# Optimization experiments

Measured on AMD Instinct MI355X. Metric: run time of the kernel, lower is better.

The kernel has to match this reference:

```python
import jax, jax.numpy as jnp
import numpy as np

B = 128   # batch_size (number of trees / source tweets)
H = 100   # tweet_out_size == GRU hidden == GAT feature dim


def _gru_layer(x, h0, Wih, Whh, bih, bhh):
    # x: [T, N, D] time-major; PyTorch GRU cell math
    def step(h, xt):
        gi = xt @ Wih.T + bih
        gh = h @ Whh.T + bhh
        ir, iz, in_ = jnp.split(gi, 3, axis=-1)
        hr, hz, hn = jnp.split(gh, 3, axis=-1)
        r = jax.nn.sigmoid(ir + hr)
        z = jax.nn.sigmoid(iz + hz)
        n = jnp.tanh(in_ + r * hn)
        h = (1.0 - z) * n + z * h
        return h, h
    hT, ys = jax.lax.scan(step, h0, x)
    return ys, hT


def _gru2(x, h0, Wih0, Whh0, bih0, bhh0, Wih1, Whh1, bih1, bhh1):
    y0, _ = _gru_layer(x, h0[0], Wih0, Whh0, bih0, bhh0)
    _, h1 = _gru_layer(y0, h0[1], Wih1, Whh1, bih1, bhh1)
    return h1  # final hidden of top layer: [N, H]


def _gat(x, ei, W, a_src, a_dst, b, heads, outc, concat):
    # PyG GATConv (eval mode, add_self_loops=True, leaky_relu slope 0.2)
    N = x.shape[0]
    loops = jnp.arange(N, dtype=ei.dtype)
    src = jnp.concatenate([ei[0], loops])
    dst = jnp.concatenate([ei[1], loops])
    h = (x @ W.T).reshape(N, heads, outc)           # [N, H, C]
    es = (h * a_src).sum(-1)                         # [N, H]
    ed = (h * a_dst).sum(-1)
    e = jax.nn.leaky_relu(es[src] + ed[dst], negative_slope=0.2)  # [E, H]
    m = jax.lax.stop_gradient(jax.ops.segment_max(e, dst, num_segments=N))
    ee = jnp.exp(e - m[dst])
    s = jax.ops.segment_sum(ee, dst, num_segments=N)
    alpha = ee / s[dst]
    out = jax.ops.segment_sum(h[src] * alpha[:, :, None], dst, num_segments=N)
    out = out.reshape(N, heads * outc) if concat else out.mean(axis=1)
    return out + b


def _forward(fl, user_text, gnode, gei, tnode, tei, idx):
    (user_feats, h0g, h0t, temb,
     gWih0, gWhh0, gbih0, gbhh0, gWih1, gWhh1, gbih1, gbhh1,
     tWih0, tWhh0, tbih0, tbhh0, tWih1, tWhh1, tbih1, tbhh1,
     uW1, ub1, uW2, ub2,
     gc1W, gc1as, gc1ad, gc1b, gc2W, gc2as, gc2ad, gc2b,
     tc1W, tc1as, tc1ad, tc1b, tc2W, tc2as, tc2ad, tc2b,
     fcW, fcb) = fl
    # --- graphGAT branch ---
    ue = jax.nn.relu(user_feats @ uW1.T + ub1) @ uW2.T + ub2        # [Nu, 100]
    ge = temb[gnode].transpose(1, 0, 2)                              # [T, Ntg, 100]
    hg = _gru2(ge, h0g, gWih0, gWhh0, gbih0, gbhh0, gWih1, gWhh1, gbih1, gbhh1)
    xg = jnp.concatenate([hg[:B], ue, hg[B:]], axis=0)               # [Ng, 100]
    xg = jax.nn.relu(_gat(xg, gei, gc1W, gc1as, gc1ad, gc1b, 8, 64, True))
    xg = jax.nn.relu(_gat(xg, gei, gc2W, gc2as, gc2ad, gc2b, 1, 100, False))
    # --- TreeGAT branch ---
    te = temb[tnode].transpose(1, 0, 2)                              # [T, Ntree, 100]
    ht = _gru2(te, h0t, tWih0, tWhh0, tbih0, tbhh0, tWih1, tWhh1, tbih1, tbhh1)
    xt = ht.at[:B].set(xg[:B])                                       # root rows <- user_root_embed
    xt = jax.nn.relu(_gat(xt, tei, tc1W, tc1as, tc1ad, tc1b, 8, 100, True))
    xt = jax.nn.relu(_gat(xt, tei, tc2W, tc2as, tc2ad, tc2b, 1, 100, False))
    # --- scatter_mean over trees + classifier ---
    ssum = jax.ops.segment_sum(xt, idx, num_segments=B)
    cnt = jax.ops.segment_sum(jnp.ones((xt.shape[0],), xt.dtype), idx, num_segments=B)
    mean = ssum / jnp.maximum(cnt, 1.0)[:, None]
    return mean @ fcW.T + fcb                                        # [B, 4]


def setup_inputs():
    key = jax.random.key(0)
    it = iter(jax.random.split(key, 60))
    def nrm(shape, s):
        return (jax.random.normal(next(it), shape) * s).astype(jnp.float32)
    Ntg, Nu, Ntree = 10000, 20000, 30000
    Ng = Ntg + Nu
    Eg, Et, V, T = 200000, 60000, 50000, 20
    inp = {}
    inp["user_text"] = jax.random.randint(next(it), (Nu, 10), 0, 1000)
    inp["user_feats"] = nrm((Nu, 9), 1.0)
    inp["graph_node_features"] = jax.random.randint(next(it), (Ntg, T), 0, V)
    inp["graph_edge_index"] = jax.random.randint(next(it), (2, Eg), 0, Ng)
    inp["merged_tree_feature"] = jax.random.randint(next(it), (Ntree, T), 0, V)
    inp["merged_tree_edge_index"] = jax.random.randint(next(it), (2, Et), 0, Ntree)
    inp["indices"] = jax.random.randint(next(it), (Ntree,), 0, B)
    inp["h0_graph"] = nrm((2, Ntg, H), 1.0)
    inp["h0_tree"] = nrm((2, Ntree, H), 1.0)
    inp["tweet_emb"] = nrm((V, H), 1.0)
    s = 0.1
    for p in ("g", "t"):
        for l in ("0", "1"):
            inp[p + "Wih" + l] = nrm((3 * H, H), s)
            inp[p + "Whh" + l] = nrm((3 * H, H), s)
            inp[p + "bih" + l] = jnp.zeros((3 * H,), jnp.float32)
            inp[p + "bhh" + l] = jnp.zeros((3 * H,), jnp.float32)
    inp["uW1"] = nrm((100, 9), s);    inp["ub1"] = jnp.zeros((100,), jnp.float32)
    inp["uW2"] = nrm((100, 100), s);  inp["ub2"] = jnp.zeros((100,), jnp.float32)
    inp["gc1W"] = nrm((512, 100), s); inp["gc1as"] = nrm((8, 64), s); inp["gc1ad"] = nrm((8, 64), s); inp["gc1b"] = jnp.zeros((512,), jnp.float32)
    inp["gc2W"] = nrm((100, 512), s); inp["gc2as"] = nrm((1, 100), s); inp["gc2ad"] = nrm((1, 100), s); inp["gc2b"] = jnp.zeros((100,), jnp.float32)
    inp["tc1W"] = nrm((800, 100), s); inp["tc1as"] = nrm((8, 100), s); inp["tc1ad"] = nrm((8, 100), s); inp["tc1b"] = jnp.zeros((800,), jnp.float32)
    inp["tc2W"] = nrm((100, 800), s); inp["tc2as"] = nrm((1, 100), s); inp["tc2ad"] = nrm((1, 100), s); inp["tc2b"] = jnp.zeros((100,), jnp.float32)
    inp["fcW"] = nrm((4, 100), s);    inp["fcb"] = jnp.zeros((4,), jnp.float32)
    return inp


def reference(user_text, user_feats, graph_node_features, graph_edge_index,
              merged_tree_feature, merged_tree_edge_index, indices,
              h0_graph, h0_tree, tweet_emb,
              gWih0, gWhh0, gbih0, gbhh0, gWih1, gWhh1, gbih1, gbhh1,
              tWih0, tWhh0, tbih0, tbhh0, tWih1, tWhh1, tbih1, tbhh1,
              uW1, ub1, uW2, ub2,
              gc1W, gc1as, gc1ad, gc1b, gc2W, gc2as, gc2ad, gc2b,
              tc1W, tc1as, tc1ad, tc1b, tc2W, tc2as, tc2ad, tc2b,
              fcW, fcb):
    fl = (user_feats, h0_graph, h0_tree, tweet_emb,
          gWih0, gWhh0, gbih0, gbhh0, gWih1, gWhh1, gbih1, gbhh1,
          tWih0, tWhh0, tbih0, tbhh0, tWih1, tWhh1, tbih1, tbhh1,
          uW1, ub1, uW2, ub2,
          gc1W, gc1as, gc1ad, gc1b, gc2W, gc2as, gc2ad, gc2b,
          tc1W, tc1as, tc1ad, tc1b, tc2W, tc2as, tc2ad, tc2b,
          fcW, fcb)
    return _forward(fl, user_text, graph_node_features, graph_edge_index,
                    merged_tree_feature, merged_tree_edge_index, indices)
```

## Files before the change

kernel.cpp:

```cpp
#include <hip/hip_runtime.h>

#define NB    128
#define HD    100
#define NU    20000
#define NTG   10000
#define NTREE 30000
#define NG    30000
#define TT    20
#define EG    200000
#define ET    60000
#define VOC   50000

#define ESTR2 448
#define WROWS 336

typedef unsigned short u16;
typedef unsigned int   u32;
typedef __attribute__((ext_vector_type(8))) short short8;
typedef __attribute__((ext_vector_type(4))) float floatx4;

__device__ __forceinline__ float sigmoidf_(float x) {
    return __fdividef(1.f, 1.f + __expf(-x));
}
__device__ __forceinline__ float tanhf_(float x) {
    return 1.f - __fdividef(2.f, __expf(2.f * x) + 1.f);
}
__device__ __forceinline__ u16 f2bf(float f) {
    u32 u = __float_as_uint(f);
    u32 r = (u + 0x7fffu + ((u >> 16) & 1u)) >> 16;
    return (u16)r;
}
__device__ __forceinline__ u16 f2bf_c(float f) {
    u32 r;
    asm("v_cvt_pk_bf16_f32 %0, %1, %2" : "=v"(r) : "v"(f), "v"(f));
    return (u16)r;
}
__device__ __forceinline__ float bf2f(u16 h) {
    return __uint_as_float(((u32)h) << 16);
}

struct GruProb {
    const u16*   Etab;
    const int*   nodes;
    const float* h0;
    const u16*   Whh0;
    const u16*   Wih1;
    const u16*   Whh1;
    u16*         hout;
    int          M;
};

__global__ __launch_bounds__(448, 2) void gru_fused9(GruProb Pg, GruProb Pt, int gblocks)
{
    const bool isg = (int)blockIdx.x < gblocks;
    const GruProb P = isg ? Pg : Pt;
    const int bx = isg ? blockIdx.x : blockIdx.x - gblocks;
    const int M  = P.M;
    const int m0 = bx * 32;

    __shared__ u16 H0[2][32 * 128];
    __shared__ u16 H1[2][32 * 128];
    __shared__ int NID[TT * 32];

    const int tid  = threadIdx.x;
    const int w    = tid >> 6, lane = tid & 63;
    const int fr   = lane & 15, quad = lane >> 4;
    const int c    = w * 16 + fr;
    const bool cok = (c < HD);

    short8 Bh0[3][4], Bx1[3][4], Bh1[3][4];
#pragma unroll
    for (int g = 0; g < 3; ++g) {
        const size_t rb = (size_t)((g * 7 + w) * 16 + fr) * 128 + quad * 8;
#pragma unroll
        for (int kk = 0; kk < 4; ++kk) {
            Bh0[g][kk] = *(const short8*)(P.Whh0 + rb + kk * 32);
            Bx1[g][kk] = *(const short8*)(P.Wih1 + rb + kk * 32);
            Bh1[g][kk] = *(const short8*)(P.Whh1 + rb + kk * 32);
        }
    }

    for (int i = tid; i < 32 * 128; i += 448) {
        H0[0][i] = 0; H0[1][i] = 0; H1[0][i] = 0; H1[1][i] = 0;
    }
    for (int i = tid; i < 32 * TT; i += 448) {
        int row = i / TT, t = i - row * TT;
        int gm = m0 + row;
        NID[t * 32 + row] = (gm < M) ? P.nodes[(size_t)gm * TT + t] : 0;
    }
    __syncthreads();
    if (tid < 32) {
        int off = 200 ^ ((tid & 7) << 4);
        *(u16*)((char*)&H0[0][0] + tid * 256 + off) = 0x3F80;
        *(u16*)((char*)&H0[1][0] + tid * 256 + off) = 0x3F80;
        *(u16*)((char*)&H1[0][0] + tid * 256 + off) = 0x3F80;
        *(u16*)((char*)&H1[1][0] + tid * 256 + off) = 0x3F80;
    }

    float h0f[2][4] = {{0.f,0.f,0.f,0.f},{0.f,0.f,0.f,0.f}};
    float h1f[2][4] = {{0.f,0.f,0.f,0.f},{0.f,0.f,0.f,0.f}};
    if (cok) {
#pragma unroll
        for (int rt = 0; rt < 2; ++rt)
#pragma unroll
        for (int r = 0; r < 4; ++r) {
            int row = rt * 16 + quad * 4 + r;
            int gm  = m0 + row;
            float v0 = 0.f, v1 = 0.f;
            if (gm < M) {
                v0 = P.h0[(size_t)gm * HD + c];
                v1 = P.h0[(size_t)(M + gm) * HD + c];
            }
            h0f[rt][r] = v0; h1f[rt][r] = v1;
            int off = (2 * c) ^ ((row & 7) << 4);
            *(u16*)((char*)&H0[0][0] + row * 256 + off) = f2bf_c(v0);
            *(u16*)((char*)&H1[0][0] + row * 256 + off) = f2bf_c(v1);
        }
    }

    u32 xlo[2][4], xhi[2][4];
    auto xpref = [&](int tn) {
        if (cok) {
#pragma unroll
            for (int rt = 0; rt < 2; ++rt)
#pragma unroll
            for (int r = 0; r < 4; ++r) {
                int row = rt * 16 + quad * 4 + r;
                int nd  = NID[tn * 32 + row];
                uint2 v = *(const uint2*)(P.Etab + (size_t)nd * ESTR2 + c * 4);
                xlo[rt][r] = v.x; xhi[rt][r] = v.y;
            }
        }
    };
    __syncthreads();
    xpref(0);

#pragma unroll
    for (int rt = 0; rt < 2; ++rt) {
        short8 a[4];
#pragma unroll
        for (int kk = 0; kk < 4; ++kk) {
            int row = rt * 16 + fr;
            int off = (kk * 64 + quad * 16) ^ ((row & 7) << 4);
            a[kk] = *(const short8*)((const char*)&H0[0][0] + row * 256 + off);
        }
        floatx4 ag[3];
#pragma unroll
        for (int g = 0; g < 3; ++g) ag[g] = (floatx4){0.f, 0.f, 0.f, 0.f};
#pragma unroll
        for (int g = 0; g < 3; ++g)
#pragma unroll
            for (int kk = 0; kk < 4; ++kk)
                ag[g] = __builtin_amdgcn_mfma_f32_16x16x32_bf16(a[kk], Bh0[g][kk], ag[g], 0, 0, 0);
        if (cok) {
#pragma unroll
            for (int r = 0; r < 4; ++r) {
                int row = rt * 16 + quad * 4 + r;
                float rr = sigmoidf_(bf2f((u16)xlo[rt][r]) + ag[0][r]);
                float zz = sigmoidf_(bf2f((u16)(xlo[rt][r] >> 16)) + ag[1][r]);
                float nn = tanhf_(bf2f((u16)xhi[rt][r]) + rr * ag[2][r]);
                float o  = (1.f - zz) * nn + zz * h0f[rt][r];
                h0f[rt][r] = o;
                *(u16*)((char*)&H0[1][0] + row * 256 + ((2 * c) ^ ((row & 7) << 4))) = f2bf_c(o);
            }
        }
    }
    __syncthreads();

    for (int r = 0; r < TT; ++r) {
        const bool doA = (r + 1 < TT);
        if (doA) xpref(r + 1);

        const char* rd0 = (const char*)&H0[(r + 1) & 1][0];
        const char* rd1 = (const char*)&H1[r & 1][0];
        char*       wr0 = (char*)&H0[r & 1][0];
        char*       wr1 = (char*)&H1[(r + 1) & 1][0];

#pragma unroll
        for (int rt = 0; rt < 2; ++rt) {
            short8 a0[4], a1[4];
#pragma unroll
            for (int kk = 0; kk < 4; ++kk) {
                int row = rt * 16 + fr;
                int off = (kk * 64 + quad * 16) ^ ((row & 7) << 4);
                a0[kk] = *(const short8*)(rd0 + row * 256 + off);
                a1[kk] = *(const short8*)(rd1 + row * 256 + off);
            }
            floatx4 rz0 = {0.f,0.f,0.f,0.f}, rz1 = {0.f,0.f,0.f,0.f};
            floatx4 xnv = {0.f,0.f,0.f,0.f}, hnv = {0.f,0.f,0.f,0.f};
#pragma unroll
            for (int kk = 0; kk < 4; ++kk)
                rz0 = __builtin_amdgcn_mfma_f32_16x16x32_bf16(a0[kk], Bx1[0][kk], rz0, 0, 0, 0);
#pragma unroll
            for (int kk = 0; kk < 4; ++kk)
                rz0 = __builtin_amdgcn_mfma_f32_16x16x32_bf16(a1[kk], Bh1[0][kk], rz0, 0, 0, 0);
#pragma unroll
            for (int kk = 0; kk < 4; ++kk)
                rz1 = __builtin_amdgcn_mfma_f32_16x16x32_bf16(a0[kk], Bx1[1][kk], rz1, 0, 0, 0);
#pragma unroll
            for (int kk = 0; kk < 4; ++kk)
                rz1 = __builtin_amdgcn_mfma_f32_16x16x32_bf16(a1[kk], Bh1[1][kk], rz1, 0, 0, 0);
#pragma unroll
            for (int kk = 0; kk < 4; ++kk)
                xnv = __builtin_amdgcn_mfma_f32_16x16x32_bf16(a0[kk], Bx1[2][kk], xnv, 0, 0, 0);
#pragma unroll
            for (int kk = 0; kk < 4; ++kk)
                hnv = __builtin_amdgcn_mfma_f32_16x16x32_bf16(a1[kk], Bh1[2][kk], hnv, 0, 0, 0);
            floatx4 ag[3];
#pragma unroll
            for (int g = 0; g < 3; ++g) ag[g] = (floatx4){0.f, 0.f, 0.f, 0.f};
            if (doA) {
#pragma unroll
                for (int g = 0; g < 3; ++g)
#pragma unroll
                    for (int kk = 0; kk < 4; ++kk)
                        ag[g] = __builtin_amdgcn_mfma_f32_16x16x32_bf16(a0[kk], Bh0[g][kk], ag[g], 0, 0, 0);
            }
            if (cok) {
#pragma unroll
                for (int r4 = 0; r4 < 4; ++r4) {
                    int row = rt * 16 + quad * 4 + r4;
                    float rr = sigmoidf_(rz0[r4]);
                    float zz = sigmoidf_(rz1[r4]);
                    float nn = tanhf_(xnv[r4] + rr * hnv[r4]);
                    float o  = (1.f - zz) * nn + zz * h1f[rt][r4];
                    h1f[rt][r4] = o;
                    *(u16*)(wr1 + row * 256 + ((2 * c) ^ ((row & 7) << 4))) = f2bf_c(o);
                }
                if (doA) {
#pragma unroll
                    for (int r4 = 0; r4 < 4; ++r4) {
                        int row = rt * 16 + quad * 4 + r4;
                        float rr = sigmoidf_(bf2f((u16)xlo[rt][r4]) + ag[0][r4]);
                        float zz = sigmoidf_(bf2f((u16)(xlo[rt][r4] >> 16)) + ag[1][r4]);
                        float nn = tanhf_(bf2f((u16)xhi[rt][r4]) + rr * ag[2][r4]);
                        float o  = (1.f - zz) * nn + zz * h0f[rt][r4];
                        h0f[rt][r4] = o;
                        *(u16*)(wr0 + row * 256 + ((2 * c) ^ ((row & 7) << 4))) = f2bf_c(o);
                    }
                }
            }
        }
        __syncthreads();
    }

    for (int i = tid; i < 32 * 128; i += 448) {
        int row = i >> 7, cc = i & 127;
        int gm = m0 + row;
        if (gm < M) {
            int off = (2 * cc) ^ ((row & 7) << 4);
            P.hout[(size_t)gm * 128 + cc] = *(const u16*)((const char*)&H1[0][0] + row * 256 + off);
        }
    }
}

#define LDST 40
__global__ __launch_bounds__(256) void gemm_mfma(
    const u16* __restrict__ A, const u16* __restrict__ B,
    float* __restrict__ Cf, u16* __restrict__ Cb,
    int M, int N, int Kt, int lda, int ldw, int ldc, int ileave)
{
    const int m0 = blockIdx.x * 64;
    if (m0 >= M) return;
    const int n0 = blockIdx.y * 64;

    __shared__ u16 Als[64 * LDST];
    __shared__ u16 Wls[64 * LDST];

    const int tid  = threadIdx.x;
    const int wave = tid >> 6, lane = tid & 63;
    const int row  = tid >> 2, part = (tid & 3) * 8;
    const int fr   = lane & 15, quad = lane >> 4;

    floatx4 acc[4];
#pragma unroll
    for (int t = 0; t < 4; ++t) acc[t] = (floatx4){0.f, 0.f, 0.f, 0.f};

    const int am = m0 + row;  const bool aok = am < M;
    const int wn = n0 + row;  const bool wok = wn < N;
    const uint4 z4 = {0u, 0u, 0u, 0u};

    for (int kk = 0; kk < Kt; ++kk) {
        uint4 av = aok ? *(const uint4*)(A + (size_t)am * lda + kk * 32 + part) : z4;
        uint4 wv = wok ? *(const uint4*)(B + (size_t)wn * ldw + kk * 32 + part) : z4;
        __syncthreads();
        *(uint4*)&Als[row * LDST + part] = av;
        *(uint4*)&Wls[row * LDST + part] = wv;
        __syncthreads();
        short8 af = *(const short8*)&Als[((wave << 4) + fr) * LDST + quad * 8];
#pragma unroll
        for (int t = 0; t < 4; ++t) {
            short8 bf = *(const short8*)&Wls[((t << 4) + fr) * LDST + quad * 8];
            acc[t] = __builtin_amdgcn_mfma_f32_16x16x32_bf16(af, bf, acc[t], 0, 0, 0);
        }
    }

    const int orow0 = m0 + (wave << 4) + quad * 4;
#pragma unroll
    for (int t = 0; t < 4; ++t) {
        int col = n0 + (t << 4) + fr;
        if (col >= N) continue;
#pragma unroll
        for (int r = 0; r < 4; ++r) {
            int mr = orow0 + r;
            if (mr >= M) continue;
            float v = acc[t][r];
            if (Cf) Cf[(size_t)mr * ldc + col] = v;
            if (Cb) {
                if (ileave) {
                    int g = col / 100, cc = col - g * 100;
                    Cb[(size_t)mr * ESTR2 + cc * 4 + g] = f2bf(v);
                } else {
                    Cb[(size_t)mr * ldc + col] = f2bf(v);
                }
            }
        }
    }
}

__global__ __launch_bounds__(256) void gemm_nt(
    const float* __restrict__ A, const float* __restrict__ W,
    const float* __restrict__ bias, float* __restrict__ C,
    int M, int N, int K, int relu)
{
    const int m0 = blockIdx.x * 64;
    const int n0 = blockIdx.y * 64;
    __shared__ float As[20][68];
    __shared__ float Ws[20][68];
    const int tid = threadIdx.x;
    const int r0 = (tid >> 4) * 4;
    const int c0 = (tid & 15) * 4;
    int sr[5], sk[5];
#pragma unroll
    for (int it = 0; it < 5; ++it) {
        int idx = tid + it * 256;
        sr[it] = idx / 20; sk[it] = idx - sr[it] * 20;
    }
    float acc[4][4];
#pragma unroll
    for (int i = 0; i < 4; ++i)
#pragma unroll
        for (int j = 0; j < 4; ++j) acc[i][j] = 0.f;
    const int nch = (K + 19) / 20;
    for (int ch = 0; ch < nch; ++ch) {
        const int k0 = ch * 20;
#pragma unroll
        for (int it = 0; it < 5; ++it) {
            int m = m0 + sr[it], k = k0 + sk[it];
            float va = 0.f, vw = 0.f;
            if (k < K) {
                if (m < M) va = A[(size_t)m * K + k];
                int n = n0 + sr[it];
                if (n < N) vw = W[(size_t)n * K + k];
            }
            As[sk[it]][sr[it]] = va;
            Ws[sk[it]][sr[it]] = vw;
        }
        __syncthreads();
#pragma unroll
        for (int kkk = 0; kkk < 20; ++kkk) {
            float4 a = *(const float4*)&As[kkk][r0];
            float4 w = *(const float4*)&Ws[kkk][c0];
            float av[4] = {a.x, a.y, a.z, a.w};
            float wv[4] = {w.x, w.y, w.z, w.w};
#pragma unroll
            for (int i = 0; i < 4; ++i)
#pragma unroll
                for (int j = 0; j < 4; ++j)
                    acc[i][j] = fmaf(av[i], wv[j], acc[i][j]);
        }
        __syncthreads();
    }
#pragma unroll
    for (int i = 0; i < 4; ++i) {
        int m = m0 + r0 + i;
        if (m >= M) continue;
#pragma unroll
        for (int j = 0; j < 4; ++j) {
            int n = n0 + c0 + j;
            if (n >= N) continue;
            float v = acc[i][j] + (bias ? bias[n] : 0.f);
            if (relu) v = fmaxf(v, 0.f);
            C[(size_t)m * N + n] = v;
        }
    }
}

__global__ void convert_pad2(const float* __restrict__ src, u16* __restrict__ dst,
                             int M, int Mp, int K, int ldk,
                             const float* __restrict__ app, int appone)
{
    int t = blockIdx.x * blockDim.x + threadIdx.x;
    if (t >= Mp * ldk) return;
    int n = t / ldk, c = t - n * ldk;
    u16 o = 0;
    if (n < M) {
        if (c < K) o = f2bf(src[(size_t)n * K + c]);
        else if (c == 100) {
            if (app) o = f2bf(app[n]);
            else if (appone) o = 0x3F80;
        }
    }
    dst[t] = o;
}

struct CvtgBatch {
    const float* src[6];
    const float* bias[6];
    u16*         dst[6];
};
#define CVTG_BLOCKS_PER_MAT 168
__global__ void convert_gru_w6(CvtgBatch B)
{
    int mat = blockIdx.x / CVTG_BLOCKS_PER_MAT;
    int t = (blockIdx.x - mat * CVTG_BLOCKS_PER_MAT) * blockDim.x + threadIdx.x;
    int rr = t >> 7, cc = t & 127;
    int g = rr / 112, r2 = rr - g * 112;
    u16 o = 0;
    if (r2 < 100) {
        int sr = g * 100 + r2;
        if (cc < 100) o = f2bf(B.src[mat][(size_t)sr * 100 + cc]);
        else if (cc == 100) o = f2bf(B.bias[mat][sr]);
    }
    B.dst[mat][t] = o;
}

__global__ void build_xg_bf(const u16* __restrict__ hgb, const float* __restrict__ ue,
                            u16* __restrict__ xgb)
{
    int t = blockIdx.x * blockDim.x + threadIdx.x;
    if (t >= NG * 128) return;
    int n = t >> 7, c = t & 127;
    u16 o = 0;
    if (n < NB)           o = hgb[n * 128 + c];
    else if (n < NB + NU) { if (c < HD) o = f2bf(ue[(size_t)(n - NB) * HD + c]); }
    else                  o = hgb[(size_t)(n - NU) * 128 + c];
    xgb[t] = o;
}

__global__ void set_roots(const float* __restrict__ src, u16* __restrict__ hb)
{
    int t = blockIdx.x * blockDim.x + threadIdx.x;
    if (t >= NB * HD) return;
    int n = t / HD, c = t - n * HD;
    hb[(size_t)n * 128 + c] = f2bf(src[t]);
}

__global__ void csr_count(const int* __restrict__ ei, int E, int N, int* __restrict__ cnt)
{
    int e = blockIdx.x * blockDim.x + threadIdx.x;
    if (e >= E + N) return;
    int dst = (e < E) ? ei[E + e] : e - E;
    atomicAdd(&cnt[dst], 1);
}

__global__ void csr_scan(const int* __restrict__ cnt, int* __restrict__ off,
                         int* __restrict__ cur, int N)
{
    __shared__ int part[256];
    const int tid = threadIdx.x;
    const int per = (N + 255) / 256;
    const int i0 = tid * per;
    const int i1 = min(i0 + per, N);
    int s = 0;
    for (int i = i0; i < i1; ++i) s += cnt[i];
    part[tid] = s;
    __syncthreads();
    for (int o = 1; o < 256; o <<= 1) {
        int u = (tid >= o) ? part[tid - o] : 0;
        __syncthreads();
        part[tid] += u;
        __syncthreads();
    }
    int base = part[tid] - s;
    for (int i = i0; i < i1; ++i) {
        off[i] = base; cur[i] = base;
        base += cnt[i];
    }
    if (tid == 255) off[N] = part[255];
}

__global__ void csr_scatter(const int* __restrict__ ei, int E, int N,
                            int* __restrict__ cur, int* __restrict__ eidx)
{
    int e = blockIdx.x * blockDim.x + threadIdx.x;
    if (e >= E + N) return;
    int dst = (e < E) ? ei[E + e] : e - E;
    int pos = atomicAdd(&cur[dst], 1);
    eidx[pos] = e;
}

__global__ void gat_es_ed(const u16* __restrict__ feat, const float* __restrict__ asrc,
                          const float* __restrict__ adst, float* __restrict__ es,
                          float* __restrict__ ed, float* __restrict__ m,
                          float* __restrict__ s, int N, int heads, int C)
{
    int gid = blockIdx.x * blockDim.x + threadIdx.x;
    if (gid >= N * heads) return;
    int n = gid / heads, hd = gid - n * heads;
    const u16* hp = feat + ((size_t)n * heads + hd) * C;
    const float* as = asrc + (size_t)hd * C;
    const float* ad = adst + (size_t)hd * C;
    float s1 = 0.f, s2 = 0.f;
    for (int c = 0; c < C; c += 4) {
        uint2 pk = *(const uint2*)(hp + c);
        float v0 = bf2f((u16)(pk.x & 0xffff)), v1 = bf2f((u16)(pk.x >> 16));
        float v2 = bf2f((u16)(pk.y & 0xffff)), v3 = bf2f((u16)(pk.y >> 16));
        s1 += v0 * as[c] + v1 * as[c + 1] + v2 * as[c + 2] + v3 * as[c + 3];
        s2 += v0 * ad[c] + v1 * ad[c + 1] + v2 * ad[c + 2] + v3 * ad[c + 3];
    }
    es[gid] = s1; ed[gid] = s2;
    m[gid] = __uint_as_float(0xFFFFFFFFu);
    s[gid] = 0.f;
}

__device__ __forceinline__ void atomic_max_f(float* addr, float v)
{
    if (v >= 0.f) atomicMax((int*)addr, __float_as_int(v));
    else          atomicMin((unsigned int*)addr, __float_as_uint(v));
}

__global__ void gat_edge_logit(const int* __restrict__ ei, int E, int N, int heads,
                               const float* __restrict__ es, const float* __restrict__ ed,
                               float* __restrict__ eb, float* __restrict__ m)
{
    int gid = blockIdx.x * blockDim.x + threadIdx.x;
    int EE = E + N;
    if (gid >= EE * heads) return;
    int idx = gid / heads, hd = gid - idx * heads;
    int src, dst;
    if (idx < E) { src = ei[idx]; dst = ei[E + idx]; } else { src = dst = idx - E; }
    float e = es[src * heads + hd] + ed[dst * heads + hd];
    e = e > 0.f ? e : 0.2f * e;
    eb[gid] = e;
    atomic_max_f(&m[dst * heads + hd], e);
}

__global__ void gat_edge_expsum(const int* __restrict__ ei, int E, int N, int heads,
                                float* __restrict__ eb, const float* __restrict__ m,
                                float* __restrict__ s)
{
    int gid = blockIdx.x * blockDim.x + threadIdx.x;
    int EE = E + N;
    if (gid >= EE * heads) return;
    int idx = gid / heads, hd = gid - idx * heads;
    int dst = (idx < E) ? ei[E + idx] : idx - E;
    float e = __expf(eb[gid] - m[dst * heads + hd]);
    eb[gid] = e;
    atomicAdd(&s[dst * heads + hd], e);
}

template<int C, int VEC>
__global__ __launch_bounds__(256) void gat_accum_csr(
    const int* __restrict__ off, const int* __restrict__ eidx,
    const int* __restrict__ ei, int E,
    const float* __restrict__ eb, const float* __restrict__ s,
    const u16* __restrict__ feat, const float* __restrict__ bias,
    float* __restrict__ outf, u16* __restrict__ outb,
    int N, int heads, int HC, int nchunk)
{
    int gt = blockIdx.x * blockDim.x + threadIdx.x;
    int w = gt >> 6, lane = gt & 63;
    int dst = w / nchunk, chunk = w - dst * nchunk;
    if (dst >= N) return;
    int c0 = chunk * 64 * VEC + lane * VEC;
    if (c0 >= HC) return;
    int hh[VEC]; float sinv[VEC], acc[VEC];
#pragma unroll
    for (int v = 0; v < VEC; ++v) {
        int c = c0 + v;
        hh[v] = c / C;
        sinv[v] = __fdividef(1.f, s[dst * heads + hh[v]]);
        acc[v] = 0.f;
    }
    int e0 = off[dst], e1 = off[dst + 1];
    for (int p = e0; p < e1; ++p) {
        int j = eidx[p];
        int src = (j < E) ? ei[j] : (j - E);
        const u16* frp = feat + (size_t)src * HC + c0;
        float fv[VEC];
        if (VEC == 4) {
            uint2 pk = *(const uint2*)frp;
            fv[0] = bf2f((u16)(pk.x & 0xffff)); fv[1] = bf2f((u16)(pk.x >> 16));
            fv[2] = bf2f((u16)(pk.y & 0xffff)); fv[3] = bf2f((u16)(pk.y >> 16));
        } else {
            u32 pk = *(const u32*)frp;
            fv[0] = bf2f((u16)(pk & 0xffff)); fv[1] = bf2f((u16)(pk >> 16));
        }
#pragma unroll
        for (int v = 0; v < VEC; ++v)
            acc[v] += fv[v] * eb[(size_t)j * heads + hh[v]] * sinv[v];
    }
#pragma unroll
    for (int v = 0; v < VEC; ++v) {
        int c = c0 + v;
        float o = fmaxf(acc[v] + bias[c], 0.f);
        if (outf) outf[(size_t)dst * HC + c] = o;
        if (outb) outb[(size_t)dst * HC + c] = f2bf(o);
    }
}

__global__ void scatter_mean_accum(const float* __restrict__ x, const int* __restrict__ idx,
                                   float* __restrict__ ssum, float* __restrict__ cnt)
{
    int t = blockIdx.x * blockDim.x + threadIdx.x;
    if (t >= NTREE * HD) return;
    int n = t / HD, c = t - n * HD;
    int b = idx[n];
    atomicAdd(&ssum[b * HD + c], x[t]);
    if (c == 0) atomicAdd(&cnt[b], 1.f);
}

__global__ void fc_out(const float* __restrict__ ssum, const float* __restrict__ cnt,
                       const float* __restrict__ W, const float* __restrict__ b,
                       float* __restrict__ out)
{
    int t = threadIdx.x;
    int bb = t >> 2, j = t & 3;
    float inv = __fdividef(1.f, fmaxf(cnt[bb], 1.f));
    float acc = b[j];
    for (int k = 0; k < HD; ++k) acc += ssum[bb * HD + k] * inv * W[j * HD + k];
    out[t] = acc;
}

extern "C" void kernel_launch(void* const* d_in, const int* in_sizes, int n_in,
                              void* d_out, int out_size, void* d_ws, size_t ws_size,
                              hipStream_t stream)
{
    const float* user_feats = (const float*)d_in[1];
    const int*   gnf        = (const int*)d_in[2];
    const int*   gei        = (const int*)d_in[3];
    const int*   tnf        = (const int*)d_in[4];
    const int*   tei        = (const int*)d_in[5];
    const int*   indices    = (const int*)d_in[6];
    const float* h0g        = (const float*)d_in[7];
    const float* h0t        = (const float*)d_in[8];
    const float* temb       = (const float*)d_in[9];
    const float* gW[2][4] = {{(const float*)d_in[10], (const float*)d_in[11], (const float*)d_in[12], (const float*)d_in[13]},
                             {(const float*)d_in[14], (const float*)d_in[15], (const float*)d_in[16], (const float*)d_in[17]}};
    const float* tW[2][4] = {{(const float*)d_in[18], (const float*)d_in[19], (const float*)d_in[20], (const float*)d_in[21]},
                             {(const float*)d_in[22], (const float*)d_in[23], (const float*)d_in[24], (const float*)d_in[25]}};
    const float* uW1 = (const float*)d_in[26]; const float* ub1 = (const float*)d_in[27];
    const float* uW2 = (const float*)d_in[28]; const float* ub2 = (const float*)d_in[29];
    const float* gc1W = (const float*)d_in[30]; const float* gc1as = (const float*)d_in[31];
    const float* gc1ad = (const float*)d_in[32]; const float* gc1b = (const float*)d_in[33];
    const float* gc2W = (const float*)d_in[34]; const float* gc2as = (const float*)d_in[35];
    const float* gc2ad = (const float*)d_in[36]; const float* gc2b = (const float*)d_in[37];
    const float* tc1W = (const float*)d_in[38]; const float* tc1as = (const float*)d_in[39];
    const float* tc1ad = (const float*)d_in[40]; const float* tc1b = (const float*)d_in[41];
    const float* tc2W = (const float*)d_in[42]; const float* tc2as = (const float*)d_in[43];
    const float* tc2ad = (const float*)d_in[44]; const float* tc2b = (const float*)d_in[45];
    const float* fcW = (const float*)d_in[46]; const float* fcb = (const float*)d_in[47];
    float* out = (float*)d_out;

    char* ws = (char*)d_ws;
    const size_t NEED = 226500000;
    if (ws_size < NEED) return;

    float* XGF    = (float*)(ws + 0);
    u16*   TEMB_B = (u16*)(ws + 12000000);
    u16*   ETAB_G = (u16*)(ws + 25000000);
    u16*   ETAB_T = (u16*)(ws + 70000000);
    u16*   GH1B   = (u16*)(ws + 115000000);
    u16*   TH1B   = (u16*)(ws + 117600000);
    float* UE     = (float*)(ws + 125300000);
    float* HID    = (float*)(ws + 133400000);
    u16*   WARENA = (u16*)(ws + 141500000);
    int*   GOFF   = (int*)(ws + 142700000);
    int*   GCUR   = (int*)(ws + 142900000);
    int*   GCNT   = (int*)(ws + 143100000);
    int*   GEIDX  = (int*)(ws + 143300000);
    int*   TOFF   = (int*)(ws + 144300000);
    int*   TCUR   = (int*)(ws + 144500000);
    int*   TCNT   = (int*)(ws + 144700000);
    int*   TEIDX  = (int*)(ws + 144900000);
    float* ESB    = (float*)(ws + 145300000);
    float* EDB    = (float*)(ws + 146300000);
    float* MB     = (float*)(ws + 147300000);
    float* SB     = (float*)(ws + 148300000);
    float* EBB    = (float*)(ws + 149300000);
    float* SSUM   = (float*)(ws + 156700000);
    float* SCNT   = (float*)(ws + 156800000);
    u16*   XG_B   = (u16*)(ws + 157000000);
    u16*   GFEAT1 = (u16*)(ws + 165000000);
    u16*   GOUT1B = (u16*)(ws + 25000000);
    u16*   GFEAT2 = (u16*)(ws + 56000000);
    u16*   TFEAT1 = (u16*)(ws + 25000000);
    u16*   TOUT1B = (u16*)(ws + 74000000);
    u16*   TFEAT2 = (u16*)(ws + 123000000);
    float* XOUT2  = (float*)(ws + 157000000);

    u16* gWHH0 = WARENA + 0;
    u16* gWIH1 = WARENA + 43008;
    u16* gWHH1 = WARENA + 86016;
    u16* tWHH0 = WARENA + 129024;
    u16* tWIH1 = WARENA + 172032;
    u16* tWHH1 = WARENA + 215040;
    u16* W_IH0A = WARENA + 258048;
    u16* W_IH0B = WARENA + 299008;
    u16* W_G1  = WARENA + 339968;
    u16* W_G2  = WARENA + 442368;

    auto cvt = [&](const float* src, u16* dst, int M, int Mp, int K, int ldk,
                   const float* app = nullptr, int appone = 0) {
        convert_pad2<<<((size_t)Mp * ldk + 255) / 256, 256, 0, stream>>>(
            src, dst, M, Mp, K, ldk, app, appone);
    };
    auto mfma = [&](const u16* A, int lda, const u16* W, int ldw,
                    float* Cf, u16* Cb, int ldc, int M, int N, int Kt, int ileave = 0) {
        dim3 grid((M + 63) / 64, (N + 63) / 64, 1);
        gemm_mfma<<<grid, 256, 0, stream>>>(A, W, Cf, Cb, M, N, Kt, lda, ldw, ldc, ileave);
    };
    auto csr_build = [&](const int* ei, int E, int N, int* cnt, int* off, int* cur, int* eidx) {
        hipMemsetAsync(cnt, 0, (size_t)N * 4, stream);
        csr_count<<<(E + N + 255) / 256, 256, 0, stream>>>(ei, E, N, cnt);
        csr_scan<<<1, 256, 0, stream>>>(cnt, off, cur, N);
        csr_scatter<<<(E + N + 255) / 256, 256, 0, stream>>>(ei, E, N, cur, eidx);
    };
    auto gat_pre = [&](const u16* feat, int N, int heads, int C,
                       const float* asrc, const float* adst, const int* ei, int E) {
        gat_es_ed<<<(N * heads + 255) / 256, 256, 0, stream>>>(
            feat, asrc, adst, ESB, EDB, MB, SB, N, heads, C);
        int EE = E + N;
        gat_edge_logit<<<(EE * heads + 255) / 256, 256, 0, stream>>>(ei, E, N, heads, ESB, EDB, EBB, MB);
        gat_edge_expsum<<<(EE * heads + 255) / 256, 256, 0, stream>>>(ei, E, N, heads, EBB, MB, SB);
    };

    {
        dim3 g1((NU + 63) / 64, (HD + 63) / 64, 1);
        gemm_nt<<<g1, 256, 0, stream>>>(user_feats, uW1, ub1, HID, NU, HD, 9, 1);
        gemm_nt<<<g1, 256, 0, stream>>>(HID, uW2, ub2, UE, NU, HD, HD, 0);
    }

    cvt(temb, TEMB_B, VOC, VOC, HD, 128, nullptr, 1);
    {
        CvtgBatch B;
        B.src[0] = gW[0][1]; B.bias[0] = gW[0][3]; B.dst[0] = gWHH0;
        B.src[1] = gW[1][0]; B.bias[1] = gW[1][2]; B.dst[1] = gWIH1;
        B.src[2] = gW[1][1]; B.bias[2] = gW[1][3]; B.dst[2] = gWHH1;
        B.src[3] = tW[0][1]; B.bias[3] = tW[0][3]; B.dst[3] = tWHH0;
        B.src[4] = tW[1][0]; B.bias[4] = tW[1][2]; B.dst[4] = tWIH1;
        B.src[5] = tW[1][1]; B.bias[5] = tW[1][3]; B.dst[5] = tWHH1;
        convert_gru_w6<<<6 * CVTG_BLOCKS_PER_MAT, 256, 0, stream>>>(B);
    }
    cvt(gW[0][0], W_IH0A, 300, 320, HD, 128, gW[0][2]);
    cvt(tW[0][0], W_IH0B, 300, 320, HD, 128, tW[0][2]);
    mfma(TEMB_B, 128, W_IH0A, 128, nullptr, ETAB_G, ESTR2, VOC, 300, 4, 1);
    mfma(TEMB_B, 128, W_IH0B, 128, nullptr, ETAB_T, ESTR2, VOC, 300, 4, 1);

    csr_build(gei, EG, NG, GCNT, GOFF, GCUR, GEIDX);
    csr_build(tei, ET, NTREE, TCNT, TOFF, TCUR, TEIDX);

    {
        GruProb Pg = { ETAB_G, gnf, h0g, gWHH0, gWIH1, gWHH1, GH1B, NTG };
        GruProb Pt = { ETAB_T, tnf, h0t, tWHH0, tWIH1, tWHH1, TH1B, NTREE };
        int gblk = (NTG + 31) / 32;
        int tblk = (NTREE + 31) / 32;
        gru_fused9<<<gblk + tblk, 448, 0, stream>>>(Pg, Pt, gblk);
    }

    build_xg_bf<<<(NG * 128 + 255) / 256, 256, 0, stream>>>(GH1B, UE, XG_B);
    cvt(gc1W, W_G1, 512, 512, HD, 128);
    cvt(gc2W, W_G2, 100, 100, 512, 512);
    {
        mfma(XG_B, 128, W_G1, 128, nullptr, GFEAT1, 512, NG, 512, 4);
        gat_pre(GFEAT1, NG, 8, 64, gc1as, gc1ad, gei, EG);
        int waves = NG * 2;
        gat_accum_csr<64, 4><<<(waves + 3) / 4, 256, 0, stream>>>(
            GOFF, GEIDX, gei, EG, EBB, SB, GFEAT1, gc1b, nullptr, GOUT1B, NG, 8, 512, 2);
    }
    {
        mfma(GOUT1B, 512, W_G2, 512, nullptr, GFEAT2, 100, NG, 100, 16);
        gat_pre(GFEAT2, NG, 1, 100, gc2as, gc2ad, gei, EG);
        int waves = NG;
        gat_accum_csr<100, 2><<<(waves + 3) / 4, 256, 0, stream>>>(
            GOFF, GEIDX, gei, EG, EBB, SB, GFEAT2, gc2b, XGF, nullptr, NG, 1, 100, 1);
    }

    set_roots<<<(NB * HD + 255) / 256, 256, 0, stream>>>(XGF, TH1B);
    cvt(tc1W, W_G1, 800, 800, HD, 128);
    cvt(tc2W, W_G2, 100, 100, 800, 800);
    {
        mfma(TH1B, 128, W_G1, 128, nullptr, TFEAT1, 800, NTREE, 800, 4);
        gat_pre(TFEAT1, NTREE, 8, 100, tc1as, tc1ad, tei, ET);
        int waves = NTREE * 4;
        gat_accum_csr<100, 4><<<(waves + 3) / 4, 256, 0, stream>>>(
            TOFF, TEIDX, tei, ET, EBB, SB, TFEAT1, tc1b, nullptr, TOUT1B, NTREE, 8, 800, 4);
    }
    {
        mfma(TOUT1B, 800, W_G2, 800, nullptr, TFEAT2, 100, NTREE, 100, 25);
        gat_pre(TFEAT2, NTREE, 1, 100, tc2as, tc2ad, tei, ET);
        int waves = NTREE;
        gat_accum_csr<100, 2><<<(waves + 3) / 4, 256, 0, stream>>>(
            TOFF, TEIDX, tei, ET, EBB, SB, TFEAT2, tc2b, XOUT2, nullptr, NTREE, 1, 100, 1);
    }

    hipMemsetAsync(SSUM, 0, (size_t)NB * HD * 4, stream);
    hipMemsetAsync(SCNT, 0, (size_t)NB * 4, stream);
    scatter_mean_accum<<<(NTREE * HD + 255) / 256, 256, 0, stream>>>(XOUT2, indices, SSUM, SCNT);
    fc_out<<<1, 512, 0, stream>>>(SSUM, SCNT, fcW, fcb, out);
}
```

Measured before the change: 1.669 ms.

## Fold log2e into GRU weights, batch etab GEMM and CSR builds

Pre-scales the GRU gate weights and biases by log2(e) (2·log2(e) for the candidate gate) so the sigmoid and tanh can use a raw exp2 instead of exp, and rewrites the state update as nn + z*(h - nn). The input-projection weights are laid out pre-interleaved so a dedicated gemm_etab kernel handles both the graph and tree embedding tables in one launch with direct stores, with no per-element divide or modulo. The two CSR builds are merged into paired count, scan and scatter kernels that share a single memset. This removes several launches and some ALU work in the latency-bound recurrence, at the cost of a workspace layout change and small bf16 rounding differences from the scaled weights.

```diff
diff --git a/kernel.cpp b/kernel.cpp
--- a/kernel.cpp
+++ b/kernel.cpp
@@ -13,17 +13,19 @@
 
 #define ESTR2 448
 #define WROWS 336
+#define LOG2E  1.4426950408889634f
+#define LOG2E2 2.8853900817779268f
 
 typedef unsigned short u16;
 typedef unsigned int   u32;
 typedef __attribute__((ext_vector_type(8))) short short8;
 typedef __attribute__((ext_vector_type(4))) float floatx4;
 
-__device__ __forceinline__ float sigmoidf_(float x) {
-    return __fdividef(1.f, 1.f + __expf(-x));
-}
-__device__ __forceinline__ float tanhf_(float x) {
-    return 1.f - __fdividef(2.f, __expf(2.f * x) + 1.f);
+__device__ __forceinline__ float sigmoid2_(float y) {
+    return __fdividef(1.f, 1.f + __builtin_amdgcn_exp2f(-y));
+}
+__device__ __forceinline__ float tanh2_(float y) {
+    return 1.f - __fdividef(2.f, __builtin_amdgcn_exp2f(y) + 1.f);
 }
 __device__ __forceinline__ u16 f2bf(float f) {
     u32 u = __float_as_uint(f);
@@ -50,7 +52,7 @@
     int          M;
 };
 
-__global__ __launch_bounds__(448, 2) void gru_fused9(GruProb Pg, GruProb Pt, int gblocks)
+__global__ __launch_bounds__(448, 2) void gru_fused10(GruProb Pg, GruProb Pt, int gblocks)
 {
     const bool isg = (int)blockIdx.x < gblocks;
     const GruProb P = isg ? Pg : Pt;
@@ -156,10 +158,10 @@
 #pragma unroll
             for (int r = 0; r < 4; ++r) {
                 int row = rt * 16 + quad * 4 + r;
-                float rr = sigmoidf_(bf2f((u16)xlo[rt][r]) + ag[0][r]);
-                float zz = sigmoidf_(bf2f((u16)(xlo[rt][r] >> 16)) + ag[1][r]);
-                float nn = tanhf_(bf2f((u16)xhi[rt][r]) + rr * ag[2][r]);
-                float o  = (1.f - zz) * nn + zz * h0f[rt][r];
+                float rr = sigmoid2_(bf2f((u16)xlo[rt][r]) + ag[0][r]);
+                float zz = sigmoid2_(bf2f((u16)(xlo[rt][r] >> 16)) + ag[1][r]);
+                float nn = tanh2_(bf2f((u16)xhi[rt][r]) + rr * ag[2][r]);
+                float o  = nn + zz * (h0f[rt][r] - nn);
                 h0f[rt][r] = o;
                 *(u16*)((char*)&H0[1][0] + row * 256 + ((2 * c) ^ ((row & 7) << 4))) = f2bf_c(o);
             }
@@ -220,10 +222,10 @@
 #pragma unroll
                 for (int r4 = 0; r4 < 4; ++r4) {
                     int row = rt * 16 + quad * 4 + r4;
-                    float rr = sigmoidf_(rz0[r4]);
-                    float zz = sigmoidf_(rz1[r4]);
-                    float nn = tanhf_(xnv[r4] + rr * hnv[r4]);
-                    float o  = (1.f - zz) * nn + zz * h1f[rt][r4];
+                    float rr = sigmoid2_(rz0[r4]);
+                    float zz = sigmoid2_(rz1[r4]);
+                    float nn = tanh2_(xnv[r4] + rr * hnv[r4]);
+                    float o  = nn + zz * (h1f[rt][r4] - nn);
                     h1f[rt][r4] = o;
                     *(u16*)(wr1 + row * 256 + ((2 * c) ^ ((row & 7) << 4))) = f2bf_c(o);
                 }
@@ -231,10 +233,10 @@
 #pragma unroll
                     for (int r4 = 0; r4 < 4; ++r4) {
                         int row = rt * 16 + quad * 4 + r4;
-                        float rr = sigmoidf_(bf2f((u16)xlo[rt][r4]) + ag[0][r4]);
-                        float zz = sigmoidf_(bf2f((u16)(xlo[rt][r4] >> 16)) + ag[1][r4]);
-                        float nn = tanhf_(bf2f((u16)xhi[rt][r4]) + rr * ag[2][r4]);
-                        float o  = (1.f - zz) * nn + zz * h0f[rt][r4];
+                        float rr = sigmoid2_(bf2f((u16)xlo[rt][r4]) + ag[0][r4]);
+                        float zz = sigmoid2_(bf2f((u16)(xlo[rt][r4] >> 16)) + ag[1][r4]);
+                        float nn = tanh2_(bf2f((u16)xhi[rt][r4]) + rr * ag[2][r4]);
+                        float o  = nn + zz * (h0f[rt][r4] - nn);
                         h0f[rt][r4] = o;
                         *(u16*)(wr0 + row * 256 + ((2 * c) ^ ((row & 7) << 4))) = f2bf_c(o);
                     }
@@ -258,7 +260,7 @@
 __global__ __launch_bounds__(256) void gemm_mfma(
     const u16* __restrict__ A, const u16* __restrict__ B,
     float* __restrict__ Cf, u16* __restrict__ Cb,
-    int M, int N, int Kt, int lda, int ldw, int ldc, int ileave)
+    int M, int N, int Kt, int lda, int ldw, int ldc)
 {
     const int m0 = blockIdx.x * 64;
     if (m0 >= M) return;
@@ -306,15 +308,60 @@
             if (mr >= M) continue;
             float v = acc[t][r];
             if (Cf) Cf[(size_t)mr * ldc + col] = v;
-            if (Cb) {
-                if (ileave) {
-                    int g = col / 100, cc = col - g * 100;
-                    Cb[(size_t)mr * ESTR2 + cc * 4 + g] = f2bf(v);
-                } else {
-                    Cb[(size_t)mr * ldc + col] = f2bf(v);
-                }
-            }
-        }
+            if (Cb) Cb[(size_t)mr * ldc + col] = f2bf(v);
+        }
+    }
+}
+
+__global__ __launch_bounds__(256) void gemm_etab(
+    const u16* __restrict__ A, const u16* __restrict__ W0, const u16* __restrict__ W1,
+    u16* __restrict__ C0, u16* __restrict__ C1)
+{
+    const int m0 = blockIdx.x * 64;
+    const int n0 = blockIdx.y * 64;
+    const u16* B = blockIdx.z ? W1 : W0;
+    u16* Cb = blockIdx.z ? C1 : C0;
+    const int N = 400;
+
+    __shared__ u16 Als[64 * LDST];
+    __shared__ u16 Wls[64 * LDST];
+
+    const int tid  = threadIdx.x;
+    const int wave = tid >> 6, lane = tid & 63;
+    const int row  = tid >> 2, part = (tid & 3) * 8;
+    const int fr   = lane & 15, quad = lane >> 4;
+
+    floatx4 acc[4];
+#pragma unroll
+    for (int t = 0; t < 4; ++t) acc[t] = (floatx4){0.f, 0.f, 0.f, 0.f};
+
+    const int am = m0 + row;
+    const int wn = n0 + row;  const bool wok = wn < N;
+    const uint4 z4 = {0u, 0u, 0u, 0u};
+
+    for (int kk = 0; kk < 4; ++kk) {
+        uint4 av = *(const uint4*)(A + (size_t)am * 128 + kk * 32 + part);
+        uint4 wv = wok ? *(const uint4*)(B + (size_t)wn * 128 + kk * 32 + part) : z4;
+        __syncthreads();
+        *(uint4*)&Als[row * LDST + part] = av;
+        *(uint4*)&Wls[row * LDST + part] = wv;
+        __syncthreads();
+        short8 af = *(const short8*)&Als[((wave << 4) + fr) * LDST + quad * 8];
+#pragma unroll
+        for (int t = 0; t < 4; ++t) {
+            short8 bf = *(const short8*)&Wls[((t << 4) + fr) * LDST + quad * 8];
+            acc[t] = __builtin_amdgcn_mfma_f32_16x16x32_bf16(af, bf, acc[t], 0, 0, 0);
+        }
+    }
+
+    const int orow0 = m0 + (wave << 4) + quad * 4;
+#pragma unroll
+    for (int t = 0; t < 4; ++t) {
+        int col = n0 + (t << 4) + fr;
+        if (col >= N) continue;
+#pragma unroll
+        for (int r = 0; r < 4; ++r)
+            Cb[(size_t)(orow0 + r) * ESTR2 + col] = f2bf(acc[t][r]);
     }
 }
 
@@ -418,11 +465,36 @@
     int g = rr / 112, r2 = rr - g * 112;
     u16 o = 0;
     if (r2 < 100) {
+        float sc = (g == 2) ? LOG2E2 : LOG2E;
         int sr = g * 100 + r2;
-        if (cc < 100) o = f2bf(B.src[mat][(size_t)sr * 100 + cc]);
-        else if (cc == 100) o = f2bf(B.bias[mat][sr]);
+        if (cc < 100) o = f2bf(B.src[mat][(size_t)sr * 100 + cc] * sc);
+        else if (cc == 100) o = f2bf(B.bias[mat][sr] * sc);
     }
     B.dst[mat][t] = o;
+}
+
+__global__ void convert_ih0(const float* __restrict__ s0, const float* __restrict__ b0,
+                            u16* __restrict__ d0,
+                            const float* __restrict__ s1, const float* __restrict__ b1,
+                            u16* __restrict__ d1)
+{
+    int t = blockIdx.x * blockDim.x + threadIdx.x;
+    if (t >= 2 * 448 * 128) return;
+    int which = t / (448 * 128);
+    int tt = t - which * (448 * 128);
+    const float* s = which ? s1 : s0;
+    const float* b = which ? b1 : b0;
+    u16* d = which ? d1 : d0;
+    int j = tt >> 7, kc = tt & 127;
+    int cc = j >> 2, g = j & 3;
+    u16 o = 0;
+    if (g < 3 && cc < 100) {
+        float sc = (g == 2) ? LOG2E2 : LOG2E;
+        int sr = g * 100 + cc;
+        if (kc < 100) o = f2bf(s[(size_t)sr * 100 + kc] * sc);
+        else if (kc == 100) o = f2bf(b[sr] * sc);
+    }
+    d[tt] = o;
 }
 
 __global__ void build_xg_bf(const u16* __restrict__ hgb, const float* __restrict__ ue,
@@ -446,17 +518,29 @@
     hb[(size_t)n * 128 + c] = f2bf(src[t]);
 }
 
-__global__ void csr_count(const int* __restrict__ ei, int E, int N, int* __restrict__ cnt)
+__global__ void csr_count2(const int* __restrict__ gei, const int* __restrict__ tei,
+                           int* __restrict__ gcnt, int* __restrict__ tcnt)
 {
     int e = blockIdx.x * blockDim.x + threadIdx.x;
-    if (e >= E + N) return;
-    int dst = (e < E) ? ei[E + e] : e - E;
-    atomicAdd(&cnt[dst], 1);
-}
-
-__global__ void csr_scan(const int* __restrict__ cnt, int* __restrict__ off,
-                         int* __restrict__ cur, int N)
-{
+    const int GE = EG + NG;
+    if (e < GE) {
+        int dst = (e < EG) ? gei[EG + e] : e - EG;
+        atomicAdd(&gcnt[dst], 1);
+    } else {
+        int e2 = e - GE;
+        if (e2 >= ET + NTREE) return;
+        int dst = (e2 < ET) ? tei[ET + e2] : e2 - ET;
+        atomicAdd(&tcnt[dst], 1);
+    }
+}
+
+__global__ void csr_scan2(int* __restrict__ gcnt, int* __restrict__ goff, int* __restrict__ gcur,
+                          int* __restrict__ tcnt, int* __restrict__ toff, int* __restrict__ tcur)
+{
+    const int* cnt = blockIdx.x ? tcnt : gcnt;
+    int* off = blockIdx.x ? toff : goff;
+    int* cur = blockIdx.x ? tcur : gcur;
+    const int N = blockIdx.x ? NTREE : NG;
     __shared__ int part[256];
     const int tid = threadIdx.x;
     const int per = (N + 255) / 256;
@@ -480,14 +564,23 @@
     if (tid == 255) off[N] = part[255];
 }
 
-__global__ void csr_scatter(const int* __restrict__ ei, int E, int N,
-                            int* __restrict__ cur, int* __restrict__ eidx)
+__global__ void csr_scatter2(const int* __restrict__ gei, const int* __restrict__ tei,
+                             int* __restrict__ gcur, int* __restrict__ tcur,
+                             int* __restrict__ geidx, int* __restrict__ teidx)
 {
     int e = blockIdx.x * blockDim.x + threadIdx.x;
-    if (e >= E + N) return;
-    int dst = (e < E) ? ei[E + e] : e - E;
-    int pos = atomicAdd(&cur[dst], 1);
-    eidx[pos] = e;
+    const int GE = EG + NG;
+    if (e < GE) {
+        int dst = (e < EG) ? gei[EG + e] : e - EG;
+        int pos = atomicAdd(&gcur[dst], 1);
+        geidx[pos] = e;
+    } else {
+        int e2 = e - GE;
+        if (e2 >= ET + NTREE) return;
+        int dst = (e2 < ET) ? tei[ET + e2] : e2 - ET;
+        int pos = atomicAdd(&tcur[dst], 1);
+        teidx[pos] = e2;
+    }
 }
 
 __global__ void gat_es_ed(const u16* __restrict__ feat, const float* __restrict__ asrc,
@@ -669,11 +762,11 @@
     int*   GOFF   = (int*)(ws + 142700000);
     int*   GCUR   = (int*)(ws + 142900000);
     int*   GCNT   = (int*)(ws + 143100000);
-    int*   GEIDX  = (int*)(ws + 143300000);
-    int*   TOFF   = (int*)(ws + 144300000);
-    int*   TCUR   = (int*)(ws + 144500000);
-    int*   TCNT   = (int*)(ws + 144700000);
-    int*   TEIDX  = (int*)(ws + 144900000);
+    int*   TCNT   = (int*)(ws + 143220000);
+    int*   GEIDX  = (int*)(ws + 143400000);
+    int*   TOFF   = (int*)(ws + 144400000);
+    int*   TCUR   = (int*)(ws + 144600000);
+    int*   TEIDX  = (int*)(ws + 144800000);
     float* ESB    = (float*)(ws + 145300000);
     float* EDB    = (float*)(ws + 146300000);
     float* MB     = (float*)(ws + 147300000);
@@ -690,16 +783,16 @@
     u16*   TFEAT2 = (u16*)(ws + 123000000);
     float* XOUT2  = (float*)(ws + 157000000);
 
-    u16* gWHH0 = WARENA + 0;
-    u16* gWIH1 = WARENA + 43008;
-    u16* gWHH1 = WARENA + 86016;
-    u16* tWHH0 = WARENA + 129024;
-    u16* tWIH1 = WARENA + 172032;
-    u16* tWHH1 = WARENA + 215040;
+    u16* gWHH0  = WARENA + 0;
+    u16* gWIH1  = WARENA + 43008;
+    u16* gWHH1  = WARENA + 86016;
+    u16* tWHH0  = WARENA + 129024;
+    u16* tWIH1  = WARENA + 172032;
+    u16* tWHH1  = WARENA + 215040;
     u16* W_IH0A = WARENA + 258048;
-    u16* W_IH0B = WARENA + 299008;
-    u16* W_G1  = WARENA + 339968;
-    u16* W_G2  = WARENA + 442368;
+    u16* W_IH0B = WARENA + 315392;
+    u16* W_G1   = WARENA + 372736;
+    u16* W_G2   = WARENA + 475136;
 
     auto cvt = [&](const float* src, u16* dst, int M, int Mp, int K, int ldk,
                    const float* app = nullptr, int appone = 0) {
@@ -707,15 +800,9 @@
             src, dst, M, Mp, K, ldk, app, appone);
     };
     auto mfma = [&](const u16* A, int lda, const u16* W, int ldw,
-                    float* Cf, u16* Cb, int ldc, int M, int N, int Kt, int ileave = 0) {
+                    float* Cf, u16* Cb, int ldc, int M, int N, int Kt) {
         dim3 grid((M + 63) / 64, (N + 63) / 64, 1);
-        gemm_mfma<<<grid, 256, 0, stream>>>(A, W, Cf, Cb, M, N, Kt, lda, ldw, ldc, ileave);
-    };
-    auto csr_build = [&](const int* ei, int E, int N, int* cnt, int* off, int* cur, int* eidx) {
-        hipMemsetAsync(cnt, 0, (size_t)N * 4, stream);
-        csr_count<<<(E + N + 255) / 256, 256, 0, stream>>>(ei, E, N, cnt);
-        csr_scan<<<1, 256, 0, stream>>>(cnt, off, cur, N);
-        csr_scatter<<<(E + N + 255) / 256, 256, 0, stream>>>(ei, E, N, cur, eidx);
+        gemm_mfma<<<grid, 256, 0, stream>>>(A, W, Cf, Cb, M, N, Kt, lda, ldw, ldc);
     };
     auto gat_pre = [&](const u16* feat, int N, int heads, int C,
                        const float* asrc, const float* adst, const int* ei, int E) {
@@ -743,20 +830,27 @@
         B.src[5] = tW[1][1]; B.bias[5] = tW[1][3]; B.dst[5] = tWHH1;
         convert_gru_w6<<<6 * CVTG_BLOCKS_PER_MAT, 256, 0, stream>>>(B);
     }
-    cvt(gW[0][0], W_IH0A, 300, 320, HD, 128, gW[0][2]);
-    cvt(tW[0][0], W_IH0B, 300, 320, HD, 128, tW[0][2]);
-    mfma(TEMB_B, 128, W_IH0A, 128, nullptr, ETAB_G, ESTR2, VOC, 300, 4, 1);
-    mfma(TEMB_B, 128, W_IH0B, 128, nullptr, ETAB_T, ESTR2, VOC, 300, 4, 1);
-
-    csr_build(gei, EG, NG, GCNT, GOFF, GCUR, GEIDX);
-    csr_build(tei, ET, NTREE, TCNT, TOFF, TCUR, TEIDX);
+    convert_ih0<<<(2 * 448 * 128 + 255) / 256, 256, 0, stream>>>(
+        gW[0][0], gW[0][2], W_IH0A, tW[0][0], tW[0][2], W_IH0B);
+    {
+        dim3 ge((VOC + 63) / 64, 7, 2);
+        gemm_etab<<<ge, 256, 0, stream>>>(TEMB_B, W_IH0A, W_IH0B, ETAB_G, ETAB_T);
+    }
+
+    hipMemsetAsync(GCNT, 0, 143400000 - 143100000, stream);
+    {
+        int tot = (EG + NG) + (ET + NTREE);
+        csr_count2<<<(tot + 255) / 256, 256, 0, stream>>>(gei, tei, GCNT, TCNT);
+        csr_scan2<<<2, 256, 0, stream>>>(GCNT, GOFF, GCUR, TCNT, TOFF, TCUR);
+        csr_scatter2<<<(tot + 255) / 256, 256, 0, stream>>>(gei, tei, GCUR, TCUR, GEIDX, TEIDX);
+    }
 
     {
         GruProb Pg = { ETAB_G, gnf, h0g, gWHH0, gWIH1, gWHH1, GH1B, NTG };
         GruProb Pt = { ETAB_T, tnf, h0t, tWHH0, tWIH1, tWHH1, TH1B, NTREE };
         int gblk = (NTG + 31) / 32;
         int tblk = (NTREE + 31) / 32;
-        gru_fused9<<<gblk + tblk, 448, 0, stream>>>(Pg, Pt, gblk);
+        gru_fused10<<<gblk + tblk, 448, 0, stream>>>(Pg, Pt, gblk);
     }
 
     build_xg_bf<<<(NG * 128 + 255) / 256, 256, 0, stream>>>(GH1B, UE, XG_B);
```

After: 1.547 ms. -7.3%, faster.
